# Kernel optimization log

Measured on AMD Instinct MI355X. Metric: run time of the kernel, lower is better.

## Reference

```python
import jax, jax.numpy as jnp
import numpy as np

DIM = 1024
DEPTH = 7
PAR = 8
N_NODES = 2 ** (DEPTH + 1) - 1  # 255
WIDTH = PAR * N_NODES  # 2040


def setup_inputs() -> dict:
    key = jax.random.key(0)
    k1, k2, k3, k4 = jax.random.split(key, 4)
    init_k = float(np.sqrt(1.0 / DIM))
    init_k2 = float(np.sqrt(1.0 / ((DEPTH + 1) * PAR)))
    oldx = jax.random.normal(k1, (4, 2048, DIM), dtype=jnp.float32)
    W_in = jax.random.uniform(k2, (WIDTH, DIM), jnp.float32, -init_k, init_k)
    b_in = jax.random.uniform(k3, (WIDTH,), jnp.float32, -init_k, init_k)
    W_out = jax.random.uniform(k4, (DIM, WIDTH), jnp.float32, -init_k2, init_k2)
    return {"oldx": oldx, "W_in": W_in, "b_in": b_in, "W_out": W_out}


def reference(oldx, W_in, b_in, W_out):
    x = oldx.reshape(-1, DIM)                      # [B, dim]
    B = x.shape[0]
    logits = x @ W_in.T + b_in                     # [B, width] dense GEMM over ALL nodes
    decisions = (logits > 0).astype(jnp.int32).reshape(B, PAR, N_NODES)
    acts = jax.nn.silu(logits).reshape(B, PAR, N_NODES)

    # Tree traversal: mark root, then descend DEPTH levels by each node's sign bit.
    current = jnp.zeros((B, PAR), dtype=jnp.int32)
    dmap = jax.nn.one_hot(current, N_NODES, dtype=acts.dtype)  # root node marked
    for d in range(DEPTH):
        cur_platform = 2 ** d - 1
        next_platform = 2 ** (d + 1) - 1
        moves = jnp.take_along_axis(decisions, current[..., None], axis=2)[..., 0]
        current = (current - cur_platform) * 2 + moves + next_platform
        dmap = dmap + jax.nn.one_hot(current, N_NODES, dtype=acts.dtype)

    masked = acts * jax.lax.stop_gradient(dmap)    # only depth+1 nodes per tree survive
    out = masked.reshape(B, WIDTH) @ W_out.T       # [B, dim]
    return out.reshape(oldx.shape)
```

## Files before the change

kernel.cpp:

```cpp
#include <hip/hip_runtime.h>
#include <math.h>

#define DIM 1024
#define DEPTH 7
#define PAR 8
#define N_NODES 255
#define WIDTH 2040
#define MARGIN 0.03f

#define REPLANE(p) ((((p) & 1) << 3) | ((((p) >> 1) & 1) << 4) | ((((p) >> 2) & 1) << 5))

typedef float  float2v  __attribute__((ext_vector_type(2)));
typedef _Float16 half2v __attribute__((ext_vector_type(2)));

__device__ __forceinline__ unsigned short f32_to_bf16(float f) {
    unsigned int u = __float_as_uint(f);
    u += 0x7fffu + ((u >> 16) & 1u);
    return (unsigned short)(u >> 16);
}
__device__ __forceinline__ float bf_lo(unsigned int u) { return __uint_as_float(u << 16); }
__device__ __forceinline__ float bf_hi(unsigned int u) { return __uint_as_float(u & 0xffff0000u); }

__device__ __forceinline__ half2v as_h2(unsigned int u) {
    union { unsigned int u; half2v h; } c; c.u = u; return c.h;
}
__device__ __forceinline__ unsigned int pack_h2(float a, float b) {
    union { half2v h; unsigned int u; } c;
    c.h = (half2v){(_Float16)a, (_Float16)b};
    return c.u;
}

__device__ __forceinline__ float dot2h(unsigned int a, unsigned int b, float c) {
#if __has_builtin(__builtin_amdgcn_fdot2)
    return __builtin_amdgcn_fdot2(as_h2(a), as_h2(b), c, false);
#else
    half2v ha = as_h2(a), hb = as_h2(b);
    c = fmaf((float)ha.x, (float)hb.x, c);
    return fmaf((float)ha.y, (float)hb.y, c);
#endif
}

__device__ __forceinline__ float foldK(float a, float b, int K) {
    const bool hi = (threadIdx.x & (unsigned)K) != 0;
    const float keep = hi ? b : a;
    const float send = hi ? a : b;
    return keep + __shfl_xor(send, K, 64);
}

__global__ __launch_bounds__(256) void convert_f16_kernel(
    const float* __restrict__ src, unsigned int* __restrict__ dst, int n4)
{
    int i = (int)(blockIdx.x * blockDim.x + threadIdx.x);
    if (i < n4) {
        float4 v = ((const float4*)src)[i];
        uint2 pk;
        pk.x = pack_h2(v.x, v.y);
        pk.y = pack_h2(v.z, v.w);
        ((uint2*)dst)[i] = pk;
    }
}

__global__ __launch_bounds__(256) void transpose_bf16_kernel(
    const float* __restrict__ W_out, unsigned short* __restrict__ WoT)
{
    __shared__ float tile[64][65];
    const int w0 = blockIdx.x * 64;
    const int d0 = blockIdx.y * 64;
    const int tid = (int)threadIdx.x;
    const int sub = tid & 15;
    const int grp = tid >> 4;

    #pragma unroll
    for (int pass = 0; pass < 4; ++pass) {
        const int dl = pass * 16 + grp;
        const int wl = sub * 4;
        const int w = w0 + wl;
        const int d = d0 + dl;
        float4 v = make_float4(0.f, 0.f, 0.f, 0.f);
        if (w + 3 < WIDTH) {
            v = *(const float4*)(W_out + (size_t)d * WIDTH + w);
        } else {
            float t0 = (w + 0 < WIDTH) ? W_out[(size_t)d * WIDTH + w + 0] : 0.f;
            float t1 = (w + 1 < WIDTH) ? W_out[(size_t)d * WIDTH + w + 1] : 0.f;
            float t2 = (w + 2 < WIDTH) ? W_out[(size_t)d * WIDTH + w + 2] : 0.f;
            float t3 = (w + 3 < WIDTH) ? W_out[(size_t)d * WIDTH + w + 3] : 0.f;
            v = make_float4(t0, t1, t2, t3);
        }
        tile[dl][wl + 0] = v.x; tile[dl][wl + 1] = v.y;
        tile[dl][wl + 2] = v.z; tile[dl][wl + 3] = v.w;
    }
    __syncthreads();
    #pragma unroll
    for (int pass = 0; pass < 4; ++pass) {
        const int wl = pass * 16 + grp;
        const int dl = sub * 4;
        const int w = w0 + wl;
        if (w < WIDTH) {
            unsigned int b0 = f32_to_bf16(tile[dl + 0][wl]);
            unsigned int b1 = f32_to_bf16(tile[dl + 1][wl]);
            unsigned int b2 = f32_to_bf16(tile[dl + 2][wl]);
            unsigned int b3 = f32_to_bf16(tile[dl + 3][wl]);
            uint2 pk;
            pk.x = b0 | (b1 << 16);
            pk.y = b2 | (b3 << 16);
            *(uint2*)(WoT + (size_t)w * DIM + d0 + dl) = pk;
        }
    }
}

__global__ __launch_bounds__(256) void fff_f16_kernel(
    const float* __restrict__ x,
    const float* __restrict__ W_in,
    const float* __restrict__ b_in,
    const unsigned int* __restrict__ Wh,
    const unsigned short* __restrict__ WoT,
    float* __restrict__ out,
    int B)
{
    const int wave = (int)((blockIdx.x * blockDim.x + threadIdx.x) >> 6);
    const int lane = (int)(threadIdx.x & 63);
    if (wave >= B) return;

    const float* xr = x + (size_t)wave * DIM;
    unsigned int xp[8];
    {
        float4 a0 = *(const float4*)(xr + lane * 8 + 0);
        float4 a1 = *(const float4*)(xr + lane * 8 + 4);
        float4 a2 = *(const float4*)(xr + 512 + lane * 8 + 0);
        float4 a3 = *(const float4*)(xr + 512 + lane * 8 + 4);
        xp[0] = pack_h2(a0.x, a0.y);
        xp[1] = pack_h2(a0.z, a0.w);
        xp[2] = pack_h2(a1.x, a1.y);
        xp[3] = pack_h2(a1.z, a1.w);
        xp[4] = pack_h2(a2.x, a2.y);
        xp[5] = pack_h2(a2.z, a2.w);
        xp[6] = pack_h2(a3.x, a3.y);
        xp[7] = pack_h2(a3.z, a3.w);
    }

    float2v acc2[8];
    #pragma unroll
    for (int i = 0; i < 8; ++i) acc2[i] = (float2v){0.f, 0.f};

    unsigned long long nodes = 0ULL;
    const int myp = ((lane >> 3) & 1) | (((lane >> 4) & 1) << 1) | (((lane >> 5) & 1) << 2);

    #pragma unroll 1
    for (int d = 0; d <= DEPTH; ++d) {
        int gidx[PAR];
        float partial[PAR];

        #pragma unroll
        for (int p = 0; p < PAR; ++p) {
            const int np = (int)((nodes >> (8 * p)) & 0xffULL);
            gidx[p] = p * N_NODES + np;
            const unsigned int* wr = Wh + (size_t)gidx[p] * (DIM / 2);
            const uint4 u0 = *(const uint4*)(wr + lane * 4);
            const uint4 u1 = *(const uint4*)(wr + 256 + lane * 4);
            float s = 0.f;
            s = dot2h(xp[0], u0.x, s);
            s = dot2h(xp[1], u0.y, s);
            s = dot2h(xp[2], u0.z, s);
            s = dot2h(xp[3], u0.w, s);
            s = dot2h(xp[4], u1.x, s);
            s = dot2h(xp[5], u1.y, s);
            s = dot2h(xp[6], u1.z, s);
            s = dot2h(xp[7], u1.w, s);
            partial[p] = s;
        }

        const float c01 = foldK(partial[0], partial[1], 8);
        const float c23 = foldK(partial[2], partial[3], 8);
        const float c45 = foldK(partial[4], partial[5], 8);
        const float c67 = foldK(partial[6], partial[7], 8);
        const float d0f = foldK(c01, c23, 16);
        const float d1f = foldK(c45, c67, 16);
        float e = foldK(d0f, d1f, 32);
        e += __shfl_xor(e, 1, 64);
        e += __shfl_xor(e, 2, 64);
        e += __shfl_xor(e, 4, 64);

        const int ga = (lane & 8) ? gidx[1] : gidx[0];
        const int gb = (lane & 8) ? gidx[3] : gidx[2];
        const int gc = (lane & 8) ? gidx[5] : gidx[4];
        const int gd = (lane & 8) ? gidx[7] : gidx[6];
        const int ge = (lane & 16) ? gb : ga;
        const int gf = (lane & 16) ? gd : gc;
        const int gmine = (lane & 32) ? gf : ge;
        float my = e + b_in[gmine];

        if (d < DEPTH) {
            const unsigned long long bal = __ballot(fabsf(my) < MARGIN);
            unsigned rm = 0;
            #pragma unroll
            for (int p = 0; p < PAR; ++p)
                rm |= ((unsigned)((bal >> REPLANE(p)) & 1ULL)) << p;
            if (rm) {
                const float4 fa = *(const float4*)(xr + lane * 8 + 0);
                const float4 fb = *(const float4*)(xr + lane * 8 + 4);
                const float4 fc = *(const float4*)(xr + 512 + lane * 8 + 0);
                const float4 fd = *(const float4*)(xr + 512 + lane * 8 + 4);
                while (rm) {
                    const int p = __builtin_ctz(rm); rm &= (rm - 1u);
                    const int np = (int)((nodes >> (8 * p)) & 0xffULL);
                    const int gi = p * N_NODES + np;
                    const float* wr = W_in + (size_t)gi * DIM;
                    const float4 wa = *(const float4*)(wr + lane * 8 + 0);
                    const float4 wb = *(const float4*)(wr + lane * 8 + 4);
                    const float4 wc = *(const float4*)(wr + 512 + lane * 8 + 0);
                    const float4 wd = *(const float4*)(wr + 512 + lane * 8 + 4);
                    float s = 0.f;
                    s = fmaf(fa.x, wa.x, s); s = fmaf(fa.y, wa.y, s);
                    s = fmaf(fa.z, wa.z, s); s = fmaf(fa.w, wa.w, s);
                    s = fmaf(fb.x, wb.x, s); s = fmaf(fb.y, wb.y, s);
                    s = fmaf(fb.z, wb.z, s); s = fmaf(fb.w, wb.w, s);
                    s = fmaf(fc.x, wc.x, s); s = fmaf(fc.y, wc.y, s);
                    s = fmaf(fc.z, wc.z, s); s = fmaf(fc.w, wc.w, s);
                    s = fmaf(fd.x, wd.x, s); s = fmaf(fd.y, wd.y, s);
                    s = fmaf(fd.z, wd.z, s); s = fmaf(fd.w, wd.w, s);
                    #pragma unroll
                    for (int off = 32; off >= 1; off >>= 1)
                        s += __shfl_xor(s, off, 64);
                    const float lf = s + b_in[gi];
                    my = (myp == p) ? lf : my;
                }
            }
        }

        const float act_mine = my / (1.0f + __expf(-my));
        const unsigned long long pos = __ballot(my > 0.0f);

        float act[PAR];
        #pragma unroll
        for (int p = 0; p < PAR; ++p)
            act[p] = __shfl(act_mine, REPLANE(p), 64);

        #pragma unroll
        for (int p = 0; p < PAR; ++p) {
            const unsigned short* wo = WoT + (size_t)gidx[p] * DIM;
            const uint4 u0 = *(const uint4*)(wo + lane * 8);
            const uint4 u1 = *(const uint4*)(wo + 512 + lane * 8);
            const float2v a2 = (float2v){act[p], act[p]};
            acc2[0] += a2 * (float2v){bf_lo(u0.x), bf_hi(u0.x)};
            acc2[1] += a2 * (float2v){bf_lo(u0.y), bf_hi(u0.y)};
            acc2[2] += a2 * (float2v){bf_lo(u0.z), bf_hi(u0.z)};
            acc2[3] += a2 * (float2v){bf_lo(u0.w), bf_hi(u0.w)};
            acc2[4] += a2 * (float2v){bf_lo(u1.x), bf_hi(u1.x)};
            acc2[5] += a2 * (float2v){bf_lo(u1.y), bf_hi(u1.y)};
            acc2[6] += a2 * (float2v){bf_lo(u1.z), bf_hi(u1.z)};
            acc2[7] += a2 * (float2v){bf_lo(u1.w), bf_hi(u1.w)};

            if (d < DEPTH) {
                const int np = (int)((nodes >> (8 * p)) & 0xffULL);
                const unsigned long long nn = (unsigned long long)
                    (2 * np + 1 + (int)((pos >> REPLANE(p)) & 1ULL));
                nodes = (nodes & ~(0xffULL << (8 * p))) | (nn << (8 * p));
            }
        }
    }

    float* orow = out + (size_t)wave * DIM;
    *(float4*)(orow + lane * 8 + 0) =
        make_float4(acc2[0].x, acc2[0].y, acc2[1].x, acc2[1].y);
    *(float4*)(orow + lane * 8 + 4) =
        make_float4(acc2[2].x, acc2[2].y, acc2[3].x, acc2[3].y);
    *(float4*)(orow + 512 + lane * 8 + 0) =
        make_float4(acc2[4].x, acc2[4].y, acc2[5].x, acc2[5].y);
    *(float4*)(orow + 512 + lane * 8 + 4) =
        make_float4(acc2[6].x, acc2[6].y, acc2[7].x, acc2[7].y);
}

__global__ __launch_bounds__(256) void fff_fallback_kernel(
    const float* __restrict__ x, const float* __restrict__ W_in,
    const float* __restrict__ b_in, const float* __restrict__ W_out,
    float* __restrict__ out, int B)
{
    const int wave = (int)((blockIdx.x * blockDim.x + threadIdx.x) >> 6);
    const int lane = (int)(threadIdx.x & 63);
    if (wave >= B) return;

    const float* xr = x + (size_t)wave * DIM;
    float4 x4[4];
    x4[0] = *(const float4*)(xr + lane * 8 + 0);
    x4[1] = *(const float4*)(xr + lane * 8 + 4);
    x4[2] = *(const float4*)(xr + 512 + lane * 8 + 0);
    x4[3] = *(const float4*)(xr + 512 + lane * 8 + 4);

    float acc[16];
    #pragma unroll
    for (int i = 0; i < 16; ++i) acc[i] = 0.f;
    int node[PAR];
    #pragma unroll
    for (int p = 0; p < PAR; ++p) node[p] = 0;

    for (int d = 0; d <= DEPTH; ++d) {
        #pragma unroll
        for (int p = 0; p < PAR; ++p) {
            const int gidx = p * N_NODES + node[p];
            const float* wr = W_in + (size_t)gidx * DIM;
            const float4 wa = *(const float4*)(wr + lane * 8 + 0);
            const float4 wb = *(const float4*)(wr + lane * 8 + 4);
            const float4 wc = *(const float4*)(wr + 512 + lane * 8 + 0);
            const float4 wd = *(const float4*)(wr + 512 + lane * 8 + 4);
            float s = 0.f;
            s = fmaf(x4[0].x, wa.x, s); s = fmaf(x4[0].y, wa.y, s);
            s = fmaf(x4[0].z, wa.z, s); s = fmaf(x4[0].w, wa.w, s);
            s = fmaf(x4[1].x, wb.x, s); s = fmaf(x4[1].y, wb.y, s);
            s = fmaf(x4[1].z, wb.z, s); s = fmaf(x4[1].w, wb.w, s);
            s = fmaf(x4[2].x, wc.x, s); s = fmaf(x4[2].y, wc.y, s);
            s = fmaf(x4[2].z, wc.z, s); s = fmaf(x4[2].w, wc.w, s);
            s = fmaf(x4[3].x, wd.x, s); s = fmaf(x4[3].y, wd.y, s);
            s = fmaf(x4[3].z, wd.z, s); s = fmaf(x4[3].w, wd.w, s);
            #pragma unroll
            for (int off = 32; off >= 1; off >>= 1)
                s += __shfl_xor(s, off, 64);
            const float logit = s + b_in[gidx];
            const float act = logit / (1.0f + __expf(-logit));
            #pragma unroll
            for (int k = 0; k < 2; ++k) {
                #pragma unroll
                for (int j = 0; j < 8; ++j) {
                    const int e = k * 512 + lane * 8 + j;
                    acc[k * 8 + j] = fmaf(act, W_out[(size_t)e * WIDTH + gidx], acc[k * 8 + j]);
                }
            }
            node[p] = 2 * node[p] + 1 + ((logit > 0.0f) ? 1 : 0);
        }
    }

    float* orow = out + (size_t)wave * DIM;
    *(float4*)(orow + lane * 8 + 0)       = make_float4(acc[0],  acc[1],  acc[2],  acc[3]);
    *(float4*)(orow + lane * 8 + 4)       = make_float4(acc[4],  acc[5],  acc[6],  acc[7]);
    *(float4*)(orow + 512 + lane * 8 + 0) = make_float4(acc[8],  acc[9],  acc[10], acc[11]);
    *(float4*)(orow + 512 + lane * 8 + 4) = make_float4(acc[12], acc[13], acc[14], acc[15]);
}

extern "C" void kernel_launch(void* const* d_in, const int* in_sizes, int n_in,
                              void* d_out, int out_size, void* d_ws, size_t ws_size,
                              hipStream_t stream) {
    const float* oldx  = (const float*)d_in[0];
    const float* W_in  = (const float*)d_in[1];
    const float* b_in  = (const float*)d_in[2];
    const float* W_out = (const float*)d_in[3];
    float* out = (float*)d_out;

    const int B = in_sizes[0] / DIM;

    const size_t half = (size_t)WIDTH * DIM * sizeof(unsigned short);
    const bool use_lp = (ws_size >= 2 * half) && (d_ws != nullptr);

    const int blocks = (B + 3) / 4;

    if (use_lp) {
        unsigned short* WoT = (unsigned short*)d_ws;
        unsigned int*   Wh  = (unsigned int*)((char*)d_ws + half);
        dim3 tg((WIDTH + 63) / 64, DIM / 64);
        transpose_bf16_kernel<<<tg, 256, 0, stream>>>(W_out, WoT);
        const int n4 = WIDTH * DIM / 4;
        convert_f16_kernel<<<(n4 + 255) / 256, 256, 0, stream>>>(W_in, Wh, n4);
        fff_f16_kernel<<<blocks, 256, 0, stream>>>(oldx, W_in, b_in, Wh, WoT, out, B);
    } else {
        fff_fallback_kernel<<<blocks, 256, 0, stream>>>(oldx, W_in, b_in, W_out, out, B);
    }
}
```

Baseline: 187.8 us.

## Split each row's eight trees across four waves with LDS reduction

Instead of one wave handling all eight trees for a row, each block now handles one row, and each of its four waves traverses two trees. Each wave writes its partial output to LDS, and the block sums the four partials. The aim is more parallelism per row and a shorter dependent chain of loads and shuffles per wave, so latency is hidden better. The cost is a block-wide sync, LDS traffic for the reduction, and four times as many waves loading the same x row.

Result: slower. 205.5 us (+9.4%).

```diff
diff --git a/kernel.cpp b/kernel.cpp
--- a/kernel.cpp
+++ b/kernel.cpp
@@ -7,8 +7,6 @@
 #define N_NODES 255
 #define WIDTH 2040
 #define MARGIN 0.03f
-
-#define REPLANE(p) ((((p) & 1) << 3) | ((((p) >> 1) & 1) << 4) | ((((p) >> 2) & 1) << 5))
 
 typedef float  float2v  __attribute__((ext_vector_type(2)));
 typedef _Float16 half2v __attribute__((ext_vector_type(2)));
@@ -108,7 +106,7 @@
     }
 }
 
-__global__ __launch_bounds__(256) void fff_f16_kernel(
+__global__ __launch_bounds__(256) void fff_split_kernel(
     const float* __restrict__ x,
     const float* __restrict__ W_in,
     const float* __restrict__ b_in,
@@ -117,98 +115,81 @@
     float* __restrict__ out,
     int B)
 {
-    const int wave = (int)((blockIdx.x * blockDim.x + threadIdx.x) >> 6);
+    __shared__ float red[4][DIM];
+    const int row  = (int)blockIdx.x;
+    if (row >= B) return;
+    const int wv   = (int)(threadIdx.x >> 6);
     const int lane = (int)(threadIdx.x & 63);
-    if (wave >= B) return;
-
-    const float* xr = x + (size_t)wave * DIM;
+    const int e0   = lane * 16;
+
+    const float* xr = x + (size_t)row * DIM;
     unsigned int xp[8];
     {
-        float4 a0 = *(const float4*)(xr + lane * 8 + 0);
-        float4 a1 = *(const float4*)(xr + lane * 8 + 4);
-        float4 a2 = *(const float4*)(xr + 512 + lane * 8 + 0);
-        float4 a3 = *(const float4*)(xr + 512 + lane * 8 + 4);
-        xp[0] = pack_h2(a0.x, a0.y);
-        xp[1] = pack_h2(a0.z, a0.w);
-        xp[2] = pack_h2(a1.x, a1.y);
-        xp[3] = pack_h2(a1.z, a1.w);
-        xp[4] = pack_h2(a2.x, a2.y);
-        xp[5] = pack_h2(a2.z, a2.w);
-        xp[6] = pack_h2(a3.x, a3.y);
-        xp[7] = pack_h2(a3.z, a3.w);
+        float4 a0 = *(const float4*)(xr + e0 + 0);
+        float4 a1 = *(const float4*)(xr + e0 + 4);
+        float4 a2 = *(const float4*)(xr + e0 + 8);
+        float4 a3 = *(const float4*)(xr + e0 + 12);
+        xp[0] = pack_h2(a0.x, a0.y); xp[1] = pack_h2(a0.z, a0.w);
+        xp[2] = pack_h2(a1.x, a1.y); xp[3] = pack_h2(a1.z, a1.w);
+        xp[4] = pack_h2(a2.x, a2.y); xp[5] = pack_h2(a2.z, a2.w);
+        xp[6] = pack_h2(a3.x, a3.y); xp[7] = pack_h2(a3.z, a3.w);
     }
 
     float2v acc2[8];
     #pragma unroll
     for (int i = 0; i < 8; ++i) acc2[i] = (float2v){0.f, 0.f};
 
-    unsigned long long nodes = 0ULL;
-    const int myp = ((lane >> 3) & 1) | (((lane >> 4) & 1) << 1) | (((lane >> 5) & 1) << 2);
+    const int t0 = 2 * wv, t1 = 2 * wv + 1;
+    int n0 = 0, n1 = 0;
 
     #pragma unroll 1
     for (int d = 0; d <= DEPTH; ++d) {
-        int gidx[PAR];
-        float partial[PAR];
-
-        #pragma unroll
-        for (int p = 0; p < PAR; ++p) {
-            const int np = (int)((nodes >> (8 * p)) & 0xffULL);
-            gidx[p] = p * N_NODES + np;
-            const unsigned int* wr = Wh + (size_t)gidx[p] * (DIM / 2);
-            const uint4 u0 = *(const uint4*)(wr + lane * 4);
-            const uint4 u1 = *(const uint4*)(wr + 256 + lane * 4);
-            float s = 0.f;
-            s = dot2h(xp[0], u0.x, s);
-            s = dot2h(xp[1], u0.y, s);
-            s = dot2h(xp[2], u0.z, s);
-            s = dot2h(xp[3], u0.w, s);
-            s = dot2h(xp[4], u1.x, s);
-            s = dot2h(xp[5], u1.y, s);
-            s = dot2h(xp[6], u1.z, s);
-            s = dot2h(xp[7], u1.w, s);
-            partial[p] = s;
-        }
-
-        const float c01 = foldK(partial[0], partial[1], 8);
-        const float c23 = foldK(partial[2], partial[3], 8);
-        const float c45 = foldK(partial[4], partial[5], 8);
-        const float c67 = foldK(partial[6], partial[7], 8);
-        const float d0f = foldK(c01, c23, 16);
-        const float d1f = foldK(c45, c67, 16);
-        float e = foldK(d0f, d1f, 32);
+        const int g0 = t0 * N_NODES + n0;
+        const int g1 = t1 * N_NODES + n1;
+
+        const unsigned int* wr0 = Wh + (size_t)g0 * (DIM / 2) + lane * 8;
+        const unsigned int* wr1 = Wh + (size_t)g1 * (DIM / 2) + lane * 8;
+        const uint4 ua = *(const uint4*)(wr0 + 0);
+        const uint4 ub = *(const uint4*)(wr0 + 4);
+        const uint4 va = *(const uint4*)(wr1 + 0);
+        const uint4 vb = *(const uint4*)(wr1 + 4);
+
+        float pa = 0.f, pb = 0.f;
+        pa = dot2h(xp[0], ua.x, pa); pb = dot2h(xp[0], va.x, pb);
+        pa = dot2h(xp[1], ua.y, pa); pb = dot2h(xp[1], va.y, pb);
+        pa = dot2h(xp[2], ua.z, pa); pb = dot2h(xp[2], va.z, pb);
+        pa = dot2h(xp[3], ua.w, pa); pb = dot2h(xp[3], va.w, pb);
+        pa = dot2h(xp[4], ub.x, pa); pb = dot2h(xp[4], vb.x, pb);
+        pa = dot2h(xp[5], ub.y, pa); pb = dot2h(xp[5], vb.y, pb);
+        pa = dot2h(xp[6], ub.z, pa); pb = dot2h(xp[6], vb.z, pb);
+        pa = dot2h(xp[7], ub.w, pa); pb = dot2h(xp[7], vb.w, pb);
+
+        float e = foldK(pa, pb, 32);
         e += __shfl_xor(e, 1, 64);
         e += __shfl_xor(e, 2, 64);
         e += __shfl_xor(e, 4, 64);
-
-        const int ga = (lane & 8) ? gidx[1] : gidx[0];
-        const int gb = (lane & 8) ? gidx[3] : gidx[2];
-        const int gc = (lane & 8) ? gidx[5] : gidx[4];
-        const int gd = (lane & 8) ? gidx[7] : gidx[6];
-        const int ge = (lane & 16) ? gb : ga;
-        const int gf = (lane & 16) ? gd : gc;
-        const int gmine = (lane & 32) ? gf : ge;
+        e += __shfl_xor(e, 8, 64);
+        e += __shfl_xor(e, 16, 64);
+
+        const int gmine = (lane & 32) ? g1 : g0;
         float my = e + b_in[gmine];
 
         if (d < DEPTH) {
             const unsigned long long bal = __ballot(fabsf(my) < MARGIN);
-            unsigned rm = 0;
-            #pragma unroll
-            for (int p = 0; p < PAR; ++p)
-                rm |= ((unsigned)((bal >> REPLANE(p)) & 1ULL)) << p;
-            if (rm) {
-                const float4 fa = *(const float4*)(xr + lane * 8 + 0);
-                const float4 fb = *(const float4*)(xr + lane * 8 + 4);
-                const float4 fc = *(const float4*)(xr + 512 + lane * 8 + 0);
-                const float4 fd = *(const float4*)(xr + 512 + lane * 8 + 4);
-                while (rm) {
-                    const int p = __builtin_ctz(rm); rm &= (rm - 1u);
-                    const int np = (int)((nodes >> (8 * p)) & 0xffULL);
-                    const int gi = p * N_NODES + np;
-                    const float* wr = W_in + (size_t)gi * DIM;
-                    const float4 wa = *(const float4*)(wr + lane * 8 + 0);
-                    const float4 wb = *(const float4*)(wr + lane * 8 + 4);
-                    const float4 wc = *(const float4*)(wr + 512 + lane * 8 + 0);
-                    const float4 wd = *(const float4*)(wr + 512 + lane * 8 + 4);
+            if (bal & 0x100000001ULL) {
+                const float4 fa = *(const float4*)(xr + e0 + 0);
+                const float4 fb = *(const float4*)(xr + e0 + 4);
+                const float4 fc = *(const float4*)(xr + e0 + 8);
+                const float4 fd = *(const float4*)(xr + e0 + 12);
+                #pragma unroll 1
+                for (int t = 0; t < 2; ++t) {
+                    if (!((bal >> (t * 32)) & 1ULL)) continue;
+                    const int gi = t ? g1 : g0;
+                    const float* wr = W_in + (size_t)gi * DIM + e0;
+                    const float4 wa = *(const float4*)(wr + 0);
+                    const float4 wb = *(const float4*)(wr + 4);
+                    const float4 wc = *(const float4*)(wr + 8);
+                    const float4 wd = *(const float4*)(wr + 12);
                     float s = 0.f;
                     s = fmaf(fa.x, wa.x, s); s = fmaf(fa.y, wa.y, s);
                     s = fmaf(fa.z, wa.z, s); s = fmaf(fa.w, wa.w, s);
@@ -222,52 +203,65 @@
                     for (int off = 32; off >= 1; off >>= 1)
                         s += __shfl_xor(s, off, 64);
                     const float lf = s + b_in[gi];
-                    my = (myp == p) ? lf : my;
+                    if (((lane >> 5) & 1) == t) my = lf;
                 }
             }
         }
 
         const float act_mine = my / (1.0f + __expf(-my));
         const unsigned long long pos = __ballot(my > 0.0f);
-
-        float act[PAR];
-        #pragma unroll
-        for (int p = 0; p < PAR; ++p)
-            act[p] = __shfl(act_mine, REPLANE(p), 64);
-
-        #pragma unroll
-        for (int p = 0; p < PAR; ++p) {
-            const unsigned short* wo = WoT + (size_t)gidx[p] * DIM;
-            const uint4 u0 = *(const uint4*)(wo + lane * 8);
-            const uint4 u1 = *(const uint4*)(wo + 512 + lane * 8);
-            const float2v a2 = (float2v){act[p], act[p]};
-            acc2[0] += a2 * (float2v){bf_lo(u0.x), bf_hi(u0.x)};
-            acc2[1] += a2 * (float2v){bf_lo(u0.y), bf_hi(u0.y)};
-            acc2[2] += a2 * (float2v){bf_lo(u0.z), bf_hi(u0.z)};
-            acc2[3] += a2 * (float2v){bf_lo(u0.w), bf_hi(u0.w)};
-            acc2[4] += a2 * (float2v){bf_lo(u1.x), bf_hi(u1.x)};
-            acc2[5] += a2 * (float2v){bf_lo(u1.y), bf_hi(u1.y)};
-            acc2[6] += a2 * (float2v){bf_lo(u1.z), bf_hi(u1.z)};
-            acc2[7] += a2 * (float2v){bf_lo(u1.w), bf_hi(u1.w)};
-
-            if (d < DEPTH) {
-                const int np = (int)((nodes >> (8 * p)) & 0xffULL);
-                const unsigned long long nn = (unsigned long long)
-                    (2 * np + 1 + (int)((pos >> REPLANE(p)) & 1ULL));
-                nodes = (nodes & ~(0xffULL << (8 * p))) | (nn << (8 * p));
-            }
-        }
-    }
-
-    float* orow = out + (size_t)wave * DIM;
-    *(float4*)(orow + lane * 8 + 0) =
-        make_float4(acc2[0].x, acc2[0].y, acc2[1].x, acc2[1].y);
-    *(float4*)(orow + lane * 8 + 4) =
-        make_float4(acc2[2].x, acc2[2].y, acc2[3].x, acc2[3].y);
-    *(float4*)(orow + 512 + lane * 8 + 0) =
-        make_float4(acc2[4].x, acc2[4].y, acc2[5].x, acc2[5].y);
-    *(float4*)(orow + 512 + lane * 8 + 4) =
-        make_float4(acc2[6].x, acc2[6].y, acc2[7].x, acc2[7].y);
+        const float act0 = __shfl(act_mine, 0, 64);
+        const float act1 = __shfl(act_mine, 32, 64);
+
+        const unsigned short* wo0 = WoT + (size_t)g0 * DIM + e0;
+        const unsigned short* wo1 = WoT + (size_t)g1 * DIM + e0;
+        const uint4 c0 = *(const uint4*)(wo0 + 0);
+        const uint4 c1 = *(const uint4*)(wo0 + 8);
+        const uint4 k0 = *(const uint4*)(wo1 + 0);
+        const uint4 k1 = *(const uint4*)(wo1 + 8);
+        const float2v A0 = (float2v){act0, act0};
+        const float2v A1 = (float2v){act1, act1};
+        acc2[0] += A0 * (float2v){bf_lo(c0.x), bf_hi(c0.x)};
+        acc2[1] += A0 * (float2v){bf_lo(c0.y), bf_hi(c0.y)};
+        acc2[2] += A0 * (float2v){bf_lo(c0.z), bf_hi(c0.z)};
+        acc2[3] += A0 * (float2v){bf_lo(c0.w), bf_hi(c0.w)};
+        acc2[4] += A0 * (float2v){bf_lo(c1.x), bf_hi(c1.x)};
+        acc2[5] += A0 * (float2v){bf_lo(c1.y), bf_hi(c1.y)};
+        acc2[6] += A0 * (float2v){bf_lo(c1.z), bf_hi(c1.z)};
+        acc2[7] += A0 * (float2v){bf_lo(c1.w), bf_hi(c1.w)};
+        acc2[0] += A1 * (float2v){bf_lo(k0.x), bf_hi(k0.x)};
+        acc2[1] += A1 * (float2v){bf_lo(k0.y), bf_hi(k0.y)};
+        acc2[2] += A1 * (float2v){bf_lo(k0.z), bf_hi(k0.z)};
+        acc2[3] += A1 * (float2v){bf_lo(k0.w), bf_hi(k0.w)};
+        acc2[4] += A1 * (float2v){bf_lo(k1.x), bf_hi(k1.x)};
+        acc2[5] += A1 * (float2v){bf_lo(k1.y), bf_hi(k1.y)};
+        acc2[6] += A1 * (float2v){bf_lo(k1.z), bf_hi(k1.z)};
+        acc2[7] += A1 * (float2v){bf_lo(k1.w), bf_hi(k1.w)};
+
+        if (d < DEPTH) {
+            n0 = 2 * n0 + 1 + (int)(pos & 1ULL);
+            n1 = 2 * n1 + 1 + (int)((pos >> 32) & 1ULL);
+        }
+    }
+
+    float* myred = red[wv];
+    *(float4*)(myred + e0 + 0)  = make_float4(acc2[0].x, acc2[0].y, acc2[1].x, acc2[1].y);
+    *(float4*)(myred + e0 + 4)  = make_float4(acc2[2].x, acc2[2].y, acc2[3].x, acc2[3].y);
+    *(float4*)(myred + e0 + 8)  = make_float4(acc2[4].x, acc2[4].y, acc2[5].x, acc2[5].y);
+    *(float4*)(myred + e0 + 12) = make_float4(acc2[6].x, acc2[6].y, acc2[7].x, acc2[7].y);
+    __syncthreads();
+
+    const int t = (int)threadIdx.x;
+    const float4 s0 = *(const float4*)(&red[0][t * 4]);
+    const float4 s1 = *(const float4*)(&red[1][t * 4]);
+    const float4 s2 = *(const float4*)(&red[2][t * 4]);
+    const float4 s3 = *(const float4*)(&red[3][t * 4]);
+    float4 r;
+    r.x = (s0.x + s1.x) + (s2.x + s3.x);
+    r.y = (s0.y + s1.y) + (s2.y + s3.y);
+    r.z = (s0.z + s1.z) + (s2.z + s3.z);
+    r.w = (s0.w + s1.w) + (s2.w + s3.w);
+    *(float4*)(out + (size_t)row * DIM + t * 4) = r;
 }
 
 __global__ __launch_bounds__(256) void fff_fallback_kernel(
@@ -349,8 +343,6 @@
     const size_t half = (size_t)WIDTH * DIM * sizeof(unsigned short);
     const bool use_lp = (ws_size >= 2 * half) && (d_ws != nullptr);
 
-    const int blocks = (B + 3) / 4;
-
     if (use_lp) {
         unsigned short* WoT = (unsigned short*)d_ws;
         unsigned int*   Wh  = (unsigned int*)((char*)d_ws + half);
@@ -358,8 +350,9 @@
         transpose_bf16_kernel<<<tg, 256, 0, stream>>>(W_out, WoT);
         const int n4 = WIDTH * DIM / 4;
         convert_f16_kernel<<<(n4 + 255) / 256, 256, 0, stream>>>(W_in, Wh, n4);
-        fff_f16_kernel<<<blocks, 256, 0, stream>>>(oldx, W_in, b_in, Wh, WoT, out, B);
+        fff_split_kernel<<<B, 256, 0, stream>>>(oldx, W_in, b_in, Wh, WoT, out, B);
     } else {
+        const int blocks = (B + 3) / 4;
         fff_fallback_kernel<<<blocks, 256, 0, stream>>>(oldx, W_in, b_in, W_out, out, B);
     }
 }
```
